# Optimization experiments

Hardware: AMD Instinct MI355X
Metric: run time of the kernel (lower is better)

The kernel has to match this reference:

```python
import jax, jax.numpy as jnp
import numpy as np

D_MODEL, D_STATE, D_CONV, EXPAND = 1024, 16, 4, 2
D_INNER = EXPAND * D_MODEL
B, L = 2, 1024


def setup_inputs() -> dict:
    key = jax.random.key(0)
    ks = jax.random.split(key, 8)
    s = 0.02
    return {
        "x": jax.random.normal(ks[0], (B, L, D_MODEL), jnp.float32),
        "in_proj_w": jax.random.normal(ks[1], (D_MODEL, 2 * D_INNER), jnp.float32) * s,
        "in_proj_b": jnp.zeros((2 * D_INNER,), jnp.float32),
        "conv_w": jax.random.normal(ks[2], (D_INNER, 1, D_CONV), jnp.float32) * s,
        "conv_b": jnp.zeros((D_INNER,), jnp.float32),
        "x_proj_w": jax.random.normal(ks[3], (D_INNER, 2 * D_STATE + D_INNER), jnp.float32) * s,
        "x_proj_b": jnp.zeros((2 * D_STATE + D_INNER,), jnp.float32),
        "dt_proj_w": jax.random.normal(ks[4], (D_STATE, D_INNER), jnp.float32) * s,
        "dt_proj_b": jnp.zeros((D_INNER,), jnp.float32),
        "A_log": jnp.log(jnp.tile(jnp.arange(1, D_STATE + 1, dtype=jnp.float32), (D_INNER, 1))),
        "D": jnp.ones((D_INNER,), jnp.float32),
        "out_proj_w": jax.random.normal(ks[5], (D_INNER, D_MODEL), jnp.float32) * s,
        "out_proj_b": jnp.zeros((D_MODEL,), jnp.float32),
    }


def reference(x, in_proj_w, in_proj_b, conv_w, conv_b, x_proj_w, x_proj_b,
              dt_proj_w, dt_proj_b, A_log, D, out_proj_w, out_proj_b):
    # x: (B, L, d_model)
    xz = x @ in_proj_w + in_proj_b                      # (B, L, 2*d_inner)
    xc, z = jnp.split(xz, 2, axis=-1)
    # causal depthwise conv1d (pad left by d_conv-1 == torch pad then slice [:L])
    xt = jnp.transpose(xc, (0, 2, 1))                   # (B, d_inner, L)
    xt = jax.lax.conv_general_dilated(
        xt, conv_w, window_strides=(1,), padding=[(D_CONV - 1, 0)],
        dimension_numbers=("NCH", "OIH", "NCH"),
        feature_group_count=D_INNER) + conv_b[None, :, None]
    xs = jax.nn.silu(jnp.transpose(xt, (0, 2, 1)))      # (B, L, d_inner)
    proj = xs @ x_proj_w + x_proj_b                     # (B, L, 2*d_state + d_inner)
    dt, Bp, Cp = jnp.split(proj, [D_STATE, 2 * D_STATE], axis=-1)
    # selective scan (log-cumsum parallel form, faithful to source)
    dt = jax.nn.softplus(dt @ dt_proj_w + dt_proj_b)    # (B, L, d_inner)
    A = -jnp.exp(A_log)                                 # (d_inner, d_state)
    dA = jnp.exp(dt[..., None] * A[None, None])         # (B, L, d_inner, d_state)
    dB = dt[..., None] * Bp[:, :, None, :]              # (B, L, d_inner, d_state)
    log_dA = jnp.log(dA + 1e-8)
    prefix = jnp.cumsum(log_dA, axis=1)
    prefix_shift = jnp.pad(prefix[:, :-1], ((0, 0), (1, 0), (0, 0), (0, 0)))
    dBx = dB * xs[..., None]
    h = jnp.cumsum(jnp.exp(prefix_shift) * dBx, axis=1)  # (B, L, d_inner, d_state)
    y = (h * Cp[..., None]).sum(-1)                     # (B, L, d_inner)
    y = y + xs * D
    y = y * jax.nn.silu(z)
    return y @ out_proj_w + out_proj_b                  # (B, L, d_model)
```

## Files before the change

kernel.cpp:

```cpp
#include <hip/hip_runtime.h>

#define DI 2048
#define DM 1024
#define DS 16
#define LEN 1024
#define NB 2
#define NROWS (NB * LEN)
#define NPROJ (2 * DS + DI)
#define NPROJ_PAD 2176
#define N_XZ (2 * DI)
#define CH_R 64
#define NCH (LEN / CH_R)
#define TOTCH (NB * NCH)

using bf16x8 = __attribute__((ext_vector_type(8))) short;
using f32x4  = __attribute__((ext_vector_type(4))) float;

__device__ __forceinline__ unsigned short f32_bf16(float f) {
  unsigned int u = __float_as_uint(f);
  u += 0x7fffu + ((u >> 16) & 1u);
  return (unsigned short)(u >> 16);
}
__device__ __forceinline__ float bf16_f32(unsigned short h) {
  return __uint_as_float((unsigned int)h << 16);
}

__global__ __launch_bounds__(256)
void k_transpose_bf16(const float* __restrict__ W, unsigned short* __restrict__ Wt,
                      int K, int N) {
  __shared__ float tile[32][33];
  const int n0 = blockIdx.x * 32, k0 = blockIdx.y * 32;
  const int tx = threadIdx.x & 31;
  const int ty = threadIdx.x >> 5;
#pragma unroll
  for (int j = 0; j < 32; j += 8) {
    const int n = n0 + tx, k = k0 + ty + j;
    tile[ty + j][tx] = (n < N) ? W[(size_t)k * N + n] : 0.f;
  }
  __syncthreads();
#pragma unroll
  for (int j = 0; j < 32; j += 8)
    Wt[(size_t)(n0 + ty + j) * K + (k0 + tx)] = f32_bf16(tile[tx][ty + j]);
}

__global__ __launch_bounds__(256)
void k_cast_bf16(const float* __restrict__ in, unsigned short* __restrict__ out) {
  const int i8 = (blockIdx.x * 256 + threadIdx.x) * 8;
  const float4 a = *(const float4*)(in + i8);
  const float4 b = *(const float4*)(in + i8 + 4);
  ushort4 lo, hi;
  lo.x = f32_bf16(a.x); lo.y = f32_bf16(a.y); lo.z = f32_bf16(a.z); lo.w = f32_bf16(a.w);
  hi.x = f32_bf16(b.x); hi.y = f32_bf16(b.y); hi.z = f32_bf16(b.z); hi.w = f32_bf16(b.w);
  *(ushort4*)(out + i8) = lo;
  *(ushort4*)(out + i8 + 4) = hi;
}

__global__ __launch_bounds__(256)
void k_gemm_bf(const unsigned short* __restrict__ A, int lda,
               const unsigned short* __restrict__ Bt, int ldb,
               const float* __restrict__ bias,
               float* __restrict__ C, int ldc,
               int K, int Nlog) {
  __shared__ __align__(16) unsigned short As[2][128 * 40];
  __shared__ __align__(16) unsigned short Bs[2][128 * 40];
  const int tid = threadIdx.x;
  const int m0 = blockIdx.y * 128;
  const int n0 = blockIdx.x * 128;
  const int lane = tid & 63;
  const int wid = tid >> 6;
  const int wr = (wid >> 1) * 64, wc = (wid & 1) * 64;
  const int g = lane >> 4, r = lane & 15;

  const int srow = tid >> 1;
  const int scol = (tid & 1) * 16;

  const unsigned short* Ap = A + (size_t)(m0 + srow) * lda + scol;
  const unsigned short* Bp = Bt + (size_t)(n0 + srow) * ldb + scol;
  const int swoff = srow * 40 + scol;

  f32x4 acc[4][4] = {};
  uint4 ra0, ra1, rb0, rb1;

#define LOADG(k0) do {                                                        \
    ra0 = *(const uint4*)(Ap + (k0));                                         \
    ra1 = *(const uint4*)(Ap + (k0) + 8);                                     \
    rb0 = *(const uint4*)(Bp + (k0));                                         \
    rb1 = *(const uint4*)(Bp + (k0) + 8);                                     \
  } while (0)

#define STORE(bf) do {                                                        \
    unsigned short* asw = &As[bf][swoff];                                     \
    unsigned short* bsw = &Bs[bf][swoff];                                     \
    *(uint4*)asw = ra0;                                                       \
    *(uint4*)(asw + 8) = ra1;                                                 \
    *(uint4*)bsw = rb0;                                                       \
    *(uint4*)(bsw + 8) = rb1;                                                 \
  } while (0)

#define COMPUTE(bf) do {                                                      \
    bf16x8 af[4], bfr[4];                                                     \
    _Pragma("unroll")                                                         \
    for (int i = 0; i < 4; ++i)                                               \
      af[i] = *(const bf16x8*)&As[bf][(wr + i * 16 + r) * 40 + 8 * g];        \
    _Pragma("unroll")                                                         \
    for (int j = 0; j < 4; ++j)                                               \
      bfr[j] = *(const bf16x8*)&Bs[bf][(wc + j * 16 + r) * 40 + 8 * g];       \
    _Pragma("unroll")                                                         \
    for (int i = 0; i < 4; ++i)                                               \
      _Pragma("unroll")                                                       \
      for (int j = 0; j < 4; ++j)                                             \
        acc[i][j] = __builtin_amdgcn_mfma_f32_16x16x32_bf16(af[i], bfr[j],    \
                                                            acc[i][j], 0, 0, 0);\
  } while (0)

  LOADG(0);
  STORE(0);
  __syncthreads();
  int buf = 0;
  for (int k0 = 32; k0 < K; k0 += 32) {
    LOADG(k0);
    COMPUTE(buf);
    STORE(buf ^ 1);
    __syncthreads();
    buf ^= 1;
  }
  COMPUTE(buf);

#undef LOADG
#undef STORE
#undef COMPUTE

#pragma unroll
  for (int i = 0; i < 4; ++i) {
    const int row = m0 + wr + i * 16 + 4 * g;
#pragma unroll
    for (int j = 0; j < 4; ++j) {
      const int col = n0 + wc + j * 16 + r;
      if (col < Nlog) {
        const float bv = bias[col];
#pragma unroll
        for (int q = 0; q < 4; ++q)
          C[(size_t)(row + q) * ldc + col] = acc[i][j][q] + bv;
      }
    }
  }
}

__global__ __launch_bounds__(256)
void k_conv_silu(const float* __restrict__ xz, const float* __restrict__ cw,
                 const float* __restrict__ cb, unsigned short* __restrict__ xs) {
  const int idx = blockIdx.x * 256 + threadIdx.x;
  const int d = idx & (DI - 1);
  const int row = idx >> 11;
  const int l = row & (LEN - 1);
  const float w0 = cw[d * 4], w1 = cw[d * 4 + 1], w2 = cw[d * 4 + 2], w3 = cw[d * 4 + 3];
  const float* p = xz + (size_t)row * N_XZ + d;
  float acc = cb[d] + w3 * p[0];
  if (l >= 1) acc += w2 * p[-N_XZ];
  if (l >= 2) acc += w1 * p[-2 * N_XZ];
  if (l >= 3) acc += w0 * p[-3 * N_XZ];
  xs[idx] = f32_bf16(acc / (1.f + expf(-acc)));
}

__global__ __launch_bounds__(256)
void k_dtproj(const float* __restrict__ proj, const float* __restrict__ w,
              const float* __restrict__ b, float* __restrict__ dt) {
  const int idx = blockIdx.x * 256 + threadIdx.x;
  const int d = idx & (DI - 1);
  const int row = idx >> 11;
  const float* p = proj + (size_t)row * NPROJ;
  float acc = b[d];
#pragma unroll
  for (int s = 0; s < DS; ++s) acc += p[s] * w[s * DI + d];
  dt[idx] = fmaxf(acc, 0.f) + log1pf(expf(-fabsf(acc)));
}

__global__ __launch_bounds__(256)
void k_scanA(const float* __restrict__ dt, const float* __restrict__ proj,
             const unsigned short* __restrict__ xs, const float* __restrict__ Alog,
             float* __restrict__ Ebuf, float* __restrict__ Lbuf) {
  __shared__ float bp_lds[CH_R][DS];
  const int bx = blockIdx.x;
  const int chunkg = bx >> 3;
  const int d = (bx & 7) * 256 + threadIdx.x;
  const int b = chunkg >> 4, c = chunkg & (NCH - 1);
  const int row0 = b * LEN + c * CH_R;
#pragma unroll
  for (int i = 0; i < 4; ++i) {
    const int e0 = threadIdx.x + i * 256;
    bp_lds[e0 >> 4][e0 & 15] = proj[(size_t)(row0 + (e0 >> 4)) * NPROJ + DS + (e0 & 15)];
  }
  __syncthreads();

  float a[DS], e[DS], L[DS];
#pragma unroll
  for (int s = 0; s < DS; ++s) {
    a[s] = -expf(Alog[d * DS + s]);
    e[s] = 1.f; L[s] = 0.f;
  }
#pragma unroll 4
  for (int j = 0; j < CH_R; ++j) {
    const size_t row = (size_t)(row0 + j);
    const float dtv = dt[row * DI + d];
    const float xv = bf16_f32(xs[row * DI + d]);
    const float u = dtv * xv;
#pragma unroll
    for (int q = 0; q < 4; ++q) {
      const float4 bq = *(const float4*)&bp_lds[j][q * 4];
      L[q * 4 + 0] += e[q * 4 + 0] * (u * bq.x);
      L[q * 4 + 1] += e[q * 4 + 1] * (u * bq.y);
      L[q * 4 + 2] += e[q * 4 + 2] * (u * bq.z);
      L[q * 4 + 3] += e[q * 4 + 3] * (u * bq.w);
    }
#pragma unroll
    for (int s = 0; s < DS; ++s)
      e[s] *= __expf(dtv * a[s]) + 1e-8f;
  }
  const size_t base = ((size_t)chunkg * DI + d) * DS;
#pragma unroll
  for (int q = 0; q < 4; ++q) {
    *(float4*)&Ebuf[base + q * 4] = make_float4(e[q*4], e[q*4+1], e[q*4+2], e[q*4+3]);
    *(float4*)&Lbuf[base + q * 4] = make_float4(L[q*4], L[q*4+1], L[q*4+2], L[q*4+3]);
  }
}

__global__ __launch_bounds__(256)
void k_scanB(float* __restrict__ Ebuf, float* __restrict__ Lbuf) {
  const int gid = blockIdx.x * 256 + threadIdx.x;
  const int s = gid & 15, d = (gid >> 4) & (DI - 1), b = gid >> 15;
  float scale = 1.f, H = 0.f;
#pragma unroll
  for (int c = 0; c < NCH; ++c) {
    const size_t idx = (((size_t)(b * NCH + c) * DI + d) << 4) + s;
    const float E = Ebuf[idx], Ls = Lbuf[idx];
    Ebuf[idx] = scale;
    Lbuf[idx] = H;
    H += scale * Ls;
    scale *= E;
  }
}

__global__ __launch_bounds__(256)
void k_scanC(const float* __restrict__ dt, const float* __restrict__ proj,
             const unsigned short* __restrict__ xs, const float* __restrict__ xz,
             const float* __restrict__ Alog, const float* __restrict__ Dp,
             const float* __restrict__ Ebuf, const float* __restrict__ Lbuf,
             unsigned short* __restrict__ v) {
  __shared__ float bp_lds[CH_R][DS];
  const int bx = blockIdx.x;
  const int chunkg = bx >> 3;
  const int d = (bx & 7) * 256 + threadIdx.x;
  const int b = chunkg >> 4, c = chunkg & (NCH - 1);
  const int row0 = b * LEN + c * CH_R;
#pragma unroll
  for (int i = 0; i < 4; ++i) {
    const int e0 = threadIdx.x + i * 256;
    bp_lds[e0 >> 4][e0 & 15] = proj[(size_t)(row0 + (e0 >> 4)) * NPROJ + DS + (e0 & 15)];
  }
  __syncthreads();

  const float Dd = Dp[d];
  float a[DS], e[DS], h[DS];
  const size_t base = ((size_t)chunkg * DI + d) * DS;
#pragma unroll
  for (int q = 0; q < 4; ++q) {
    const float4 ev = *(const float4*)&Ebuf[base + q * 4];
    const float4 hv = *(const float4*)&Lbuf[base + q * 4];
    e[q*4] = ev.x; e[q*4+1] = ev.y; e[q*4+2] = ev.z; e[q*4+3] = ev.w;
    h[q*4] = hv.x; h[q*4+1] = hv.y; h[q*4+2] = hv.z; h[q*4+3] = hv.w;
  }
#pragma unroll
  for (int s = 0; s < DS; ++s)
    a[s] = -expf(Alog[d * DS + s]);

#pragma unroll 4
  for (int j = 0; j < CH_R; ++j) {
    const size_t row = (size_t)(row0 + j);
    const float dtv = dt[row * DI + d];
    const float xv = bf16_f32(xs[row * DI + d]);
    const float u = dtv * xv;
#pragma unroll
    for (int q = 0; q < 4; ++q) {
      const float4 bq = *(const float4*)&bp_lds[j][q * 4];
      h[q * 4 + 0] += e[q * 4 + 0] * (u * bq.x);
      h[q * 4 + 1] += e[q * 4 + 1] * (u * bq.y);
      h[q * 4 + 2] += e[q * 4 + 2] * (u * bq.z);
      h[q * 4 + 3] += e[q * 4 + 3] * (u * bq.w);
    }
    float hs = 0.f;
#pragma unroll
    for (int s = 0; s < DS; ++s) hs += h[s];
    const float cp = proj[row * NPROJ + 2 * DS + d];
    const float z = xz[row * N_XZ + DI + d];
    const float y = cp * hs + xv * Dd;
    v[row * DI + d] = f32_bf16(y * (z / (1.f + __expf(-z))));
#pragma unroll
    for (int s = 0; s < DS; ++s)
      e[s] *= __expf(dtv * a[s]) + 1e-8f;
  }
}

extern "C" void kernel_launch(void* const* d_in, const int* in_sizes, int n_in,
                              void* d_out, int out_size, void* d_ws, size_t ws_size,
                              hipStream_t stream) {
  const float* x     = (const float*)d_in[0];
  const float* w_in  = (const float*)d_in[1];
  const float* b_in  = (const float*)d_in[2];
  const float* cw    = (const float*)d_in[3];
  const float* cb    = (const float*)d_in[4];
  const float* w_xp  = (const float*)d_in[5];
  const float* b_xp  = (const float*)d_in[6];
  const float* w_dt  = (const float*)d_in[7];
  const float* b_dt  = (const float*)d_in[8];
  const float* Alog  = (const float*)d_in[9];
  const float* Dp    = (const float*)d_in[10];
  const float* w_out = (const float*)d_in[11];
  const float* b_out = (const float*)d_in[12];
  float* out = (float*)d_out;

  char* ws = (char*)d_ws;
  unsigned short* w1t = (unsigned short*)(ws);
  unsigned short* w2t = (unsigned short*)(ws + 8388608);
  unsigned short* w3t = (unsigned short*)(ws + 17301504);
  unsigned short* xbf = (unsigned short*)(ws + 21495808);
  float* xz   = (float*)(ws + 25690112);
  unsigned short* xsb = (unsigned short*)(ws + 59244544);
  float* proj = (float*)(ws + 76021760);
  unsigned short* vb  = (unsigned short*)(ws + 93061120);
  float* dtb  = (float*)(ws);
  float* Ebuf = out;
  float* Lbuf = out + 1048576;

  const dim3 blk(256);
  k_transpose_bf16<<<dim3(4096 / 32, 1024 / 32), blk, 0, stream>>>(w_in, w1t, 1024, 4096);
  k_transpose_bf16<<<dim3(NPROJ_PAD / 32, 2048 / 32), blk, 0, stream>>>(w_xp, w2t, 2048, NPROJ);
  k_transpose_bf16<<<dim3(1024 / 32, 2048 / 32), blk, 0, stream>>>(w_out, w3t, 2048, 1024);
  k_cast_bf16<<<dim3(NROWS * DM / (256 * 8)), blk, 0, stream>>>(x, xbf);
  k_gemm_bf<<<dim3(4096 / 128, 2048 / 128), blk, 0, stream>>>(xbf, 1024, w1t, 1024, b_in, xz, 4096, 1024, 4096);
  k_conv_silu<<<dim3(NROWS * DI / 256), blk, 0, stream>>>(xz, cw, cb, xsb);
  k_gemm_bf<<<dim3(NPROJ_PAD / 128, 2048 / 128), blk, 0, stream>>>(xsb, 2048, w2t, 2048, b_xp, proj, NPROJ, 2048, NPROJ);
  k_dtproj<<<dim3(NROWS * DI / 256), blk, 0, stream>>>(proj, w_dt, b_dt, dtb);
  k_scanA<<<dim3(TOTCH * 8), blk, 0, stream>>>(dtb, proj, xsb, Alog, Ebuf, Lbuf);
  k_scanB<<<dim3(NB * DI * DS / 256), blk, 0, stream>>>(Ebuf, Lbuf);
  k_scanC<<<dim3(TOTCH * 8), blk, 0, stream>>>(dtb, proj, xsb, xz, Alog, Dp, Ebuf, Lbuf, vb);
  k_gemm_bf<<<dim3(1024 / 128, 2048 / 128), blk, 0, stream>>>(vb, 2048, w3t, 2048, b_out, out, 1024, 2048, 1024);
}
```

Baseline: 380.5 us.

## Shrink scan chunks to 16 rows and stage z as bf16

Cuts the scan chunk length from 64 to 16 rows, which quadruples the number of chunks and blocks in the scanA/scanC phases so more of the GPU runs in parallel. The chunk carry buffers grow to 16 MB each, so they move from the output buffer into workspace space that previously held xz. The conv kernel now also writes z as bf16, so scanC reads half the bytes for z. In exchange, the sequential scanB pass becomes longer and moves more carry traffic, and z loses precision.

```diff
diff --git a/kernel.cpp b/kernel.cpp
--- a/kernel.cpp
+++ b/kernel.cpp
@@ -9,7 +9,7 @@
 #define NPROJ (2 * DS + DI)
 #define NPROJ_PAD 2176
 #define N_XZ (2 * DI)
-#define CH_R 64
+#define CH_R 16
 #define NCH (LEN / CH_R)
 #define TOTCH (NB * NCH)
 
@@ -147,8 +147,9 @@
 }
 
 __global__ __launch_bounds__(256)
-void k_conv_silu(const float* __restrict__ xz, const float* __restrict__ cw,
-                 const float* __restrict__ cb, unsigned short* __restrict__ xs) {
+void k_conv_silu_z(const float* __restrict__ xz, const float* __restrict__ cw,
+                   const float* __restrict__ cb,
+                   unsigned short* __restrict__ xs, unsigned short* __restrict__ zb) {
   const int idx = blockIdx.x * 256 + threadIdx.x;
   const int d = idx & (DI - 1);
   const int row = idx >> 11;
@@ -160,6 +161,7 @@
   if (l >= 2) acc += w1 * p[-2 * N_XZ];
   if (l >= 3) acc += w0 * p[-3 * N_XZ];
   xs[idx] = f32_bf16(acc / (1.f + expf(-acc)));
+  zb[idx] = f32_bf16(p[DI]);
 }
 
 __global__ __launch_bounds__(256)
@@ -183,12 +185,11 @@
   const int bx = blockIdx.x;
   const int chunkg = bx >> 3;
   const int d = (bx & 7) * 256 + threadIdx.x;
-  const int b = chunkg >> 4, c = chunkg & (NCH - 1);
+  const int b = chunkg >> 6, c = chunkg & (NCH - 1);
   const int row0 = b * LEN + c * CH_R;
-#pragma unroll
-  for (int i = 0; i < 4; ++i) {
-    const int e0 = threadIdx.x + i * 256;
-    bp_lds[e0 >> 4][e0 & 15] = proj[(size_t)(row0 + (e0 >> 4)) * NPROJ + DS + (e0 & 15)];
+  {
+    const int t = threadIdx.x;
+    bp_lds[t >> 4][t & 15] = proj[(size_t)(row0 + (t >> 4)) * NPROJ + DS + (t & 15)];
   }
   __syncthreads();
 
@@ -229,7 +230,6 @@
   const int gid = blockIdx.x * 256 + threadIdx.x;
   const int s = gid & 15, d = (gid >> 4) & (DI - 1), b = gid >> 15;
   float scale = 1.f, H = 0.f;
-#pragma unroll
   for (int c = 0; c < NCH; ++c) {
     const size_t idx = (((size_t)(b * NCH + c) * DI + d) << 4) + s;
     const float E = Ebuf[idx], Ls = Lbuf[idx];
@@ -242,7 +242,7 @@
 
 __global__ __launch_bounds__(256)
 void k_scanC(const float* __restrict__ dt, const float* __restrict__ proj,
-             const unsigned short* __restrict__ xs, const float* __restrict__ xz,
+             const unsigned short* __restrict__ xs, const unsigned short* __restrict__ zb,
              const float* __restrict__ Alog, const float* __restrict__ Dp,
              const float* __restrict__ Ebuf, const float* __restrict__ Lbuf,
              unsigned short* __restrict__ v) {
@@ -250,12 +250,11 @@
   const int bx = blockIdx.x;
   const int chunkg = bx >> 3;
   const int d = (bx & 7) * 256 + threadIdx.x;
-  const int b = chunkg >> 4, c = chunkg & (NCH - 1);
+  const int b = chunkg >> 6, c = chunkg & (NCH - 1);
   const int row0 = b * LEN + c * CH_R;
-#pragma unroll
-  for (int i = 0; i < 4; ++i) {
-    const int e0 = threadIdx.x + i * 256;
-    bp_lds[e0 >> 4][e0 & 15] = proj[(size_t)(row0 + (e0 >> 4)) * NPROJ + DS + (e0 & 15)];
+  {
+    const int t = threadIdx.x;
+    bp_lds[t >> 4][t & 15] = proj[(size_t)(row0 + (t >> 4)) * NPROJ + DS + (t & 15)];
   }
   __syncthreads();
 
@@ -291,7 +290,7 @@
 #pragma unroll
     for (int s = 0; s < DS; ++s) hs += h[s];
     const float cp = proj[row * NPROJ + 2 * DS + d];
-    const float z = xz[row * N_XZ + DI + d];
+    const float z = bf16_f32(zb[row * DI + d]);
     const float y = cp * hs + xv * Dd;
     v[row * DI + d] = f32_bf16(y * (z / (1.f + __expf(-z))));
 #pragma unroll
@@ -325,11 +324,12 @@
   unsigned short* xbf = (unsigned short*)(ws + 21495808);
   float* xz   = (float*)(ws + 25690112);
   unsigned short* xsb = (unsigned short*)(ws + 59244544);
+  unsigned short* zbf = (unsigned short*)(ws + 67633152);
   float* proj = (float*)(ws + 76021760);
   unsigned short* vb  = (unsigned short*)(ws + 93061120);
   float* dtb  = (float*)(ws);
-  float* Ebuf = out;
-  float* Lbuf = out + 1048576;
+  float* Ebuf = (float*)(ws + 25690112);
+  float* Lbuf = (float*)(ws + 42467328);
 
   const dim3 blk(256);
   k_transpose_bf16<<<dim3(4096 / 32, 1024 / 32), blk, 0, stream>>>(w_in, w1t, 1024, 4096);
@@ -337,11 +337,11 @@
   k_transpose_bf16<<<dim3(1024 / 32, 2048 / 32), blk, 0, stream>>>(w_out, w3t, 2048, 1024);
   k_cast_bf16<<<dim3(NROWS * DM / (256 * 8)), blk, 0, stream>>>(x, xbf);
   k_gemm_bf<<<dim3(4096 / 128, 2048 / 128), blk, 0, stream>>>(xbf, 1024, w1t, 1024, b_in, xz, 4096, 1024, 4096);
-  k_conv_silu<<<dim3(NROWS * DI / 256), blk, 0, stream>>>(xz, cw, cb, xsb);
+  k_conv_silu_z<<<dim3(NROWS * DI / 256), blk, 0, stream>>>(xz, cw, cb, xsb, zbf);
   k_gemm_bf<<<dim3(NPROJ_PAD / 128, 2048 / 128), blk, 0, stream>>>(xsb, 2048, w2t, 2048, b_xp, proj, NPROJ, 2048, NPROJ);
   k_dtproj<<<dim3(NROWS * DI / 256), blk, 0, stream>>>(proj, w_dt, b_dt, dtb);
   k_scanA<<<dim3(TOTCH * 8), blk, 0, stream>>>(dtb, proj, xsb, Alog, Ebuf, Lbuf);
   k_scanB<<<dim3(NB * DI * DS / 256), blk, 0, stream>>>(Ebuf, Lbuf);
-  k_scanC<<<dim3(TOTCH * 8), blk, 0, stream>>>(dtb, proj, xsb, xz, Alog, Dp, Ebuf, Lbuf, vb);
+  k_scanC<<<dim3(TOTCH * 8), blk, 0, stream>>>(dtb, proj, xsb, zbf, Alog, Dp, Ebuf, Lbuf, vb);
   k_gemm_bf<<<dim3(1024 / 128, 2048 / 128), blk, 0, stream>>>(vb, 2048, w3t, 2048, b_out, out, 1024, 2048, 1024);
 }
```

After: 345.9 us. 9.1% less time.
